# Performance work log

Measured on AMD Instinct MI355X. Metric: run time of the kernel, lower is better.

Reference implementation:

```python
import jax, jax.numpy as jnp
import numpy as np

N_NODES = 50000
N_EDGES = 800000
N_FEAT = 16
N_BASIS = 4
GAMMA = 10.0
R_MAX = 5.0
INV_SQRT2 = 0.7071067811865476


def setup_inputs() -> dict:
    key = jax.random.key(0)
    k1, k2, k3, k4 = jax.random.split(key, 4)
    pos = jax.random.normal(k1, (N_NODES, 3), dtype=jnp.float32)
    node_features = jax.random.normal(k2, (N_NODES, N_FEAT), dtype=jnp.float32)
    # build edges with no self-loops: dst = (src + 1 + r) % N, r in [0, N-2]
    src = jax.random.randint(k3, (N_EDGES,), 0, N_NODES)
    r = jax.random.randint(k4, (N_EDGES,), 0, N_NODES - 1)
    dst = (src + 1 + r) % N_NODES
    edge_idx = jnp.stack([src, dst], axis=0).astype(jnp.int64)
    return {"pos": pos, "node_features": node_features, "edge_idx": edge_idx}


def _gaussian_basis(d):
    # d: [E] -> [E, N_BASIS]
    centers = jnp.linspace(0.0, R_MAX, N_BASIS, dtype=d.dtype)
    return jnp.exp(-GAMMA * (d[:, None] - centers[None, :]) ** 2)


def _pos_to_rep(v):
    # v: [N, 3, C] cartesian along axis -2 -> complex spherical l=1 basis,
    # returned as stacked (real, imag): [2, N, 3, C]
    x, y, z = v[..., 0, :], v[..., 1, :], v[..., 2, :]
    zero = jnp.zeros_like(z)
    real = jnp.stack([x * INV_SQRT2, z, -x * INV_SQRT2], axis=-2)
    imag = jnp.stack([-y * INV_SQRT2, zero, -y * INV_SQRT2], axis=-2)
    return jnp.stack([real, imag], axis=0)


def reference(pos, node_features, edge_idx):
    src, dst = edge_idx[0], edge_idx[1]
    disp = pos[dst] - pos[src]                      # [E, 3]
    dist = jnp.linalg.norm(disp, axis=-1)           # [E]
    bf = _gaussian_basis(dist)                      # [E, B]
    unit = disp / dist[:, None]                     # [E, 3]
    nf = node_features[dst]                         # [E, F]
    # outer products: [E, 3, B, F]
    edge_vals = (unit[:, :, None, None] * bf[:, None, :, None]
                 * nf[:, None, None, :])
    edge_vals = edge_vals.reshape(edge_vals.shape[0], 3, N_BASIS * N_FEAT)
    node_vecs = jax.ops.segment_sum(edge_vals, src, num_segments=N_NODES)  # [N,3,C]
    return _pos_to_rep(node_vecs)
```

## Files before the change

### kernel.cpp

```cpp
#include <hip/hip_runtime.h>

#define N_FEAT 16
#define N_BASIS 4
#define GAMMA 10.0f
#define R_MAX 5.0f
#define INV_SQRT2 0.70710678118654752f

#define BUCKET 50
#define CAP 1088
#define MAXB 1024
#define SC_BLOCK 512
#define SC_EDGES 4096
#define ACC_BLOCK 512

#define FXINV   (1.0f / 2097152.0f)
#define KC      (-GAMMA * 1.4426950408889634f)
#define BIAS21  21.0f

#if __has_builtin(__builtin_amdgcn_exp2f)
#define EXP2(x) __builtin_amdgcn_exp2f(x)
#else
#define EXP2(x) exp2f(x)
#endif

__global__ void bucket_scatter_kernel(const int* __restrict__ src,
                                      const int* __restrict__ dst,
                                      const float* __restrict__ pos,
                                      float4* __restrict__ pos4,
                                      int* __restrict__ gcursor,
                                      int* __restrict__ sorted,
                                      int n_edges, int nbuck, int n_nodes) {
    __shared__ int h[MAXB];
    __shared__ int cur[MAXB];
    __shared__ int gbase[MAXB];
    __shared__ int pay[SC_EDGES];

    int t = threadIdx.x;

    {
        int i = blockIdx.x * SC_BLOCK + t;
        if (i < n_nodes)
            pos4[i] = make_float4(pos[3 * i], pos[3 * i + 1], pos[3 * i + 2], 0.0f);
    }

    int base_e = blockIdx.x * SC_EDGES;
    int nloc = n_edges - base_e;
    if (nloc > SC_EDGES) nloc = SC_EDGES;

    for (int i = t; i < nbuck; i += SC_BLOCK) h[i] = 0;
    __syncthreads();

    unsigned pk[8];
    bool ok[8];
#pragma unroll
    for (int r = 0; r < 8; ++r) {
        int i = t + r * SC_BLOCK;
        ok[r] = (i < nloc);
        unsigned s = ok[r] ? (unsigned)src[base_e + i] : 0u;
        unsigned d = ok[r] ? (unsigned)dst[base_e + i] : 0u;
        pk[r] = (s << 16) | d;
        if (ok[r]) atomicAdd(&h[s / BUCKET], 1);
    }
    __syncthreads();

    if (t < 64) {
        int run = 0;
        for (int base = 0; base < nbuck; base += 64) {
            int i = base + t;
            int v = (i < nbuck) ? h[i] : 0;
            int incl = v;
            for (int off = 1; off < 64; off <<= 1) {
                int y = __shfl_up(incl, off, 64);
                if (t >= off) incl += y;
            }
            if (i < nbuck) h[i] = run + incl - v;
            run += __shfl(incl, 63, 64);
        }
    }
    __syncthreads();
    for (int i = t; i < nbuck; i += SC_BLOCK) cur[i] = h[i];
    __syncthreads();

#pragma unroll
    for (int r = 0; r < 8; ++r) {
        if (ok[r]) {
            int b = (int)((pk[r] >> 16) / BUCKET);
            int p = atomicAdd(&cur[b], 1);
            pay[p] = (int)pk[r];
        }
    }
    __syncthreads();

    for (int b = t; b < nbuck; b += SC_BLOCK) {
        int c = cur[b] - h[b];
        gbase[b] = (c > 0) ? atomicAdd(&gcursor[b], c) : 0;
    }
    __syncthreads();

    for (int i = t; i < nloc; i += SC_BLOCK) {
        unsigned P = (unsigned)pay[i];
        int b = (int)((P >> 16) / BUCKET);
        int idx = gbase[b] + (i - h[b]);
        if (idx < CAP) sorted[b * CAP + idx] = (int)P;
    }
}

__global__ __launch_bounds__(ACC_BLOCK) void accumulate_kernel(
        const float4* __restrict__ pos4,
        const float* __restrict__ nfeat,
        const int* __restrict__ sorted,
        const int* __restrict__ gcursor,
        float* __restrict__ out,
        int n_nodes) {
    __shared__ int acc[BUCKET * 192];
    __shared__ float4 spos[BUCKET];

    int b = blockIdx.x;
    int t = threadIdx.x;
    int w = t >> 6;
    int lane = t & 63;
    int g = lane >> 4;
    int f = lane & 15;
    int nbase = b * BUCKET;

    int4* accv = (int4*)acc;
    for (int i = t; i < BUCKET * 48; i += ACC_BLOCK)
        accv[i] = make_int4(0, 0, 0, 0);
    if (t < BUCKET) {
        int gn = nbase + t;
        spos[t] = (gn < n_nodes) ? pos4[gn] : make_float4(0.f, 0.f, 0.f, 0.f);
    }
    __syncthreads();

    int cnt = gcursor[b];
    if (cnt > CAP) cnt = CAP;
    const int* seg = sorted + b * CAP;

    const int stride = ACC_BLOCK / 64;
    int iters = (cnt + 3) >> 2;

    unsigned E; bool live; int sl; float4 p; float nfv; float4 ps;
    {
        int e = (w << 2) + g;
        live = (e < cnt);
        E = live ? (unsigned)seg[e] : 0u;
        int d = E & 0xFFFF;
        sl = live ? ((int)(E >> 16) - nbase) : 0;
        p = pos4[d];
        nfv = nfeat[(d << 4) + f];
        ps = spos[sl];
    }

    for (int it = w; it < iters; it += stride) {
        unsigned cE = E; bool clive = live; int csl = sl;
        float4 cp = p, cps = ps; float cnf = nfv;

        int nit = it + stride;
        if (nit < iters) {
            int e = (nit << 2) + g;
            live = (e < cnt);
            E = live ? (unsigned)seg[e] : 0u;
            int d = E & 0xFFFF;
            sl = live ? ((int)(E >> 16) - nbase) : 0;
            p = pos4[d];
            nfv = nfeat[(d << 4) + f];
            ps = spos[sl];
        }

        float dx = cp.x - cps.x, dy = cp.y - cps.y, dz = cp.z - cps.z;
        float r2 = dx * dx + dy * dy + dz * dz;
        r2 = clive ? r2 : 1.0f;
        float inv = __builtin_amdgcn_rsqf(r2);
        float dist = r2 * inv;
        float nfi = clive ? cnf * inv : 0.0f;

        int rotbase = f + (csl << 4);
        int sl192 = csl * 192;
#pragma unroll
        for (int kk = 0; kk < N_BASIS; ++kk) {
            float ck = (float)kk * (R_MAX / (N_BASIS - 1));
            float tt = dist - ck;
            float bb = EXP2(fmaf(tt * tt, KC, BIAS21));
            float val = bb * nfi;
            int* ap = acc + sl192 + ((rotbase + (kk << 4)) & 63);
            atomicAdd(ap,       (int)(dx * val));
            atomicAdd(ap + 64,  (int)(dy * val));
            atomicAdd(ap + 128, (int)(dz * val));
        }
    }

    __syncthreads();

    for (int j = w; j < BUCKET; j += stride) {
        int gn = nbase + j;
        if (gn >= n_nodes) continue;
        int rot = (lane + (j << 4)) & 63;
        int jb = j * 192;
        float x = (float)acc[jb + rot] * FXINV;
        float y = (float)acc[jb + 64 + rot] * FXINV;
        float z = (float)acc[jb + 128 + rot] * FXINV;
        size_t obase = (size_t)gn * 192 + lane;
        float* re = out + obase;
        float* im = out + (size_t)n_nodes * 192 + obase;
        float xs = x * INV_SQRT2;
        float ys = -y * INV_SQRT2;
        re[0]   = xs;
        re[64]  = z;
        re[128] = -xs;
        im[0]   = ys;
        im[64]  = 0.0f;
        im[128] = ys;
    }
}

extern "C" void kernel_launch(void* const* d_in, const int* in_sizes, int n_in,
                              void* d_out, int out_size, void* d_ws, size_t ws_size,
                              hipStream_t stream) {
    const float* pos = (const float*)d_in[0];
    const float* nfeat = (const float*)d_in[1];
    const int* edge_idx = (const int*)d_in[2];

    int n_nodes = in_sizes[0] / 3;
    int n_edges = in_sizes[2] / 2;

    const int* src = edge_idx;
    const int* dst = edge_idx + n_edges;

    float* out = (float*)d_out;
    int nbuck = (n_nodes + BUCKET - 1) / BUCKET;

    char* ws = (char*)d_ws;
    size_t o = 0;
    auto alloc = [&](size_t bytes) {
        char* p = ws + o;
        o = (o + bytes + 255) & ~(size_t)255;
        return p;
    };
    int* gcursor = (int*)alloc((size_t)nbuck * 4);
    int* sorted  = (int*)alloc((size_t)nbuck * CAP * 4);
    float4* pos4 = (float4*)alloc((size_t)n_nodes * 16);

    hipMemsetAsync(gcursor, 0, (size_t)nbuck * sizeof(int), stream);

    {
        int grid = (n_edges + SC_EDGES - 1) / SC_EDGES;
        bucket_scatter_kernel<<<grid, SC_BLOCK, 0, stream>>>(src, dst, pos, pos4,
                                                             gcursor, sorted,
                                                             n_edges, nbuck, n_nodes);
    }

    accumulate_kernel<<<nbuck, ACC_BLOCK, 0, stream>>>(pos4, nfeat, sorted, gcursor,
                                                       out, n_nodes);
}
```

Baseline: 66.81 us.

## Replace LDS fixed-point atomics with per-node local sort and register accumulation

Buckets now hold 64 nodes, so bucket indexing becomes a shift. Inside each bucket the accumulate kernel counting-sorts edges by source node in LDS. Each 16-lane group then owns one node and accumulates its 12 outputs in float registers, which removes the fixed-point LDS atomics and the quantization they introduced. The costs are load imbalance from degree variance within a wavefront (loops run to the max degree of four nodes), an extra LDS sort pass, and fewer nodes per block in flight.

```diff
diff --git a/kernel.cpp b/kernel.cpp
--- a/kernel.cpp
+++ b/kernel.cpp
@@ -6,16 +6,15 @@
 #define R_MAX 5.0f
 #define INV_SQRT2 0.70710678118654752f
 
-#define BUCKET 50
-#define CAP 1088
+#define BUCKET 64
+#define CAP 1360
 #define MAXB 1024
 #define SC_BLOCK 512
 #define SC_EDGES 4096
 #define ACC_BLOCK 512
 
-#define FXINV   (1.0f / 2097152.0f)
 #define KC      (-GAMMA * 1.4426950408889634f)
-#define BIAS21  21.0f
+#define CKD     (R_MAX / (N_BASIS - 1))
 
 #if __has_builtin(__builtin_amdgcn_exp2f)
 #define EXP2(x) __builtin_amdgcn_exp2f(x)
@@ -59,7 +58,7 @@
         unsigned s = ok[r] ? (unsigned)src[base_e + i] : 0u;
         unsigned d = ok[r] ? (unsigned)dst[base_e + i] : 0u;
         pk[r] = (s << 16) | d;
-        if (ok[r]) atomicAdd(&h[s / BUCKET], 1);
+        if (ok[r]) atomicAdd(&h[s >> 6], 1);
     }
     __syncthreads();
 
@@ -84,7 +83,7 @@
 #pragma unroll
     for (int r = 0; r < 8; ++r) {
         if (ok[r]) {
-            int b = (int)((pk[r] >> 16) / BUCKET);
+            int b = (int)(pk[r] >> 22);
             int p = atomicAdd(&cur[b], 1);
             pay[p] = (int)pk[r];
         }
@@ -99,7 +98,7 @@
 
     for (int i = t; i < nloc; i += SC_BLOCK) {
         unsigned P = (unsigned)pay[i];
-        int b = (int)((P >> 16) / BUCKET);
+        int b = (int)(P >> 22);
         int idx = gbase[b] + (i - h[b]);
         if (idx < CAP) sorted[b * CAP + idx] = (int)P;
     }
@@ -112,104 +111,140 @@
         const int* __restrict__ gcursor,
         float* __restrict__ out,
         int n_nodes) {
-    __shared__ int acc[BUCKET * 192];
+    __shared__ int spay[CAP + 64];
+    __shared__ int off[BUCKET + 1];
+    __shared__ int cnt[BUCKET];
+    __shared__ int cur[BUCKET];
     __shared__ float4 spos[BUCKET];
 
     int b = blockIdx.x;
     int t = threadIdx.x;
     int w = t >> 6;
     int lane = t & 63;
-    int g = lane >> 4;
+    int grp = lane >> 4;
     int f = lane & 15;
-    int nbase = b * BUCKET;
-
-    int4* accv = (int4*)acc;
-    for (int i = t; i < BUCKET * 48; i += ACC_BLOCK)
-        accv[i] = make_int4(0, 0, 0, 0);
+    int nbase = b << 6;
+
+    int ecnt = gcursor[b];
+    if (ecnt > CAP) ecnt = CAP;
+    const int* seg = sorted + b * CAP;
+
     if (t < BUCKET) {
+        cnt[t] = 0;
         int gn = nbase + t;
         spos[t] = (gn < n_nodes) ? pos4[gn] : make_float4(0.f, 0.f, 0.f, 0.f);
     }
     __syncthreads();
 
-    int cnt = gcursor[b];
-    if (cnt > CAP) cnt = CAP;
-    const int* seg = sorted + b * CAP;
-
-    const int stride = ACC_BLOCK / 64;
-    int iters = (cnt + 3) >> 2;
-
-    unsigned E; bool live; int sl; float4 p; float nfv; float4 ps;
-    {
-        int e = (w << 2) + g;
-        live = (e < cnt);
-        E = live ? (unsigned)seg[e] : 0u;
-        int d = E & 0xFFFF;
-        sl = live ? ((int)(E >> 16) - nbase) : 0;
-        p = pos4[d];
-        nfv = nfeat[(d << 4) + f];
-        ps = spos[sl];
-    }
-
-    for (int it = w; it < iters; it += stride) {
-        unsigned cE = E; bool clive = live; int csl = sl;
-        float4 cp = p, cps = ps; float cnf = nfv;
-
-        int nit = it + stride;
-        if (nit < iters) {
-            int e = (nit << 2) + g;
-            live = (e < cnt);
-            E = live ? (unsigned)seg[e] : 0u;
-            int d = E & 0xFFFF;
-            sl = live ? ((int)(E >> 16) - nbase) : 0;
-            p = pos4[d];
-            nfv = nfeat[(d << 4) + f];
-            ps = spos[sl];
-        }
-
-        float dx = cp.x - cps.x, dy = cp.y - cps.y, dz = cp.z - cps.z;
-        float r2 = dx * dx + dy * dy + dz * dz;
-        r2 = clive ? r2 : 1.0f;
-        float inv = __builtin_amdgcn_rsqf(r2);
-        float dist = r2 * inv;
-        float nfi = clive ? cnf * inv : 0.0f;
-
-        int rotbase = f + (csl << 4);
-        int sl192 = csl * 192;
-#pragma unroll
-        for (int kk = 0; kk < N_BASIS; ++kk) {
-            float ck = (float)kk * (R_MAX / (N_BASIS - 1));
-            float tt = dist - ck;
-            float bb = EXP2(fmaf(tt * tt, KC, BIAS21));
-            float val = bb * nfi;
-            int* ap = acc + sl192 + ((rotbase + (kk << 4)) & 63);
-            atomicAdd(ap,       (int)(dx * val));
-            atomicAdd(ap + 64,  (int)(dy * val));
-            atomicAdd(ap + 128, (int)(dz * val));
-        }
-    }
-
-    __syncthreads();
-
-    for (int j = w; j < BUCKET; j += stride) {
-        int gn = nbase + j;
-        if (gn >= n_nodes) continue;
-        int rot = (lane + (j << 4)) & 63;
-        int jb = j * 192;
-        float x = (float)acc[jb + rot] * FXINV;
-        float y = (float)acc[jb + 64 + rot] * FXINV;
-        float z = (float)acc[jb + 128 + rot] * FXINV;
-        size_t obase = (size_t)gn * 192 + lane;
-        float* re = out + obase;
-        float* im = out + (size_t)n_nodes * 192 + obase;
-        float xs = x * INV_SQRT2;
-        float ys = -y * INV_SQRT2;
-        re[0]   = xs;
-        re[64]  = z;
-        re[128] = -xs;
-        im[0]   = ys;
-        im[64]  = 0.0f;
-        im[128] = ys;
+    for (int i = t; i < ecnt; i += ACC_BLOCK)
+        atomicAdd(&cnt[((unsigned)seg[i] >> 16) & 63], 1);
+    __syncthreads();
+
+    if (t < 64) {
+        int v = cnt[t];
+        int incl = v;
+        for (int o2 = 1; o2 < 64; o2 <<= 1) {
+            int y = __shfl_up(incl, o2, 64);
+            if (t >= o2) incl += y;
+        }
+        off[t + 1] = incl;
+        if (t == 0) off[0] = 0;
+        cur[t] = incl - v;
+    }
+    __syncthreads();
+
+    for (int i = t; i < ecnt; i += ACC_BLOCK) {
+        int E = seg[i];
+        int p = atomicAdd(&cur[((unsigned)E >> 16) & 63], 1);
+        spay[p] = E;
+    }
+    __syncthreads();
+
+    for (int set = 0; set < 2; ++set) {
+        int nl = (w << 3) + (set << 2) + grp;
+        int gn = nbase + nl;
+        int myoff = off[nl];
+        int deg = off[nl + 1] - myoff;
+        float4 ps = spos[nl];
+
+        int m1 = max(deg, __shfl_xor(deg, 16, 64));
+        int maxdeg = max(m1, __shfl_xor(m1, 32, 64));
+
+        float ax0 = 0.f, ax1 = 0.f, ax2 = 0.f, ax3 = 0.f;
+        float ay0 = 0.f, ay1 = 0.f, ay2 = 0.f, ay3 = 0.f;
+        float az0 = 0.f, az1 = 0.f, az2 = 0.f, az3 = 0.f;
+
+        if (maxdeg > 0) {
+            int degm1 = (deg > 0) ? deg - 1 : 0;
+            int E1;
+            float4 p0;
+            float nf0;
+            {
+                int i0 = myoff + 0;
+                int E0 = spay[i0];
+                E1 = spay[myoff + min(1, degm1)];
+                int d0 = (deg > 0) ? (E0 & 0xFFFF) : 0;
+                p0 = pos4[d0];
+                nf0 = nfeat[(d0 << 4) + f];
+            }
+            for (int s = 0; s < maxdeg; ++s) {
+                bool clv = (s < deg);
+                float4 cp = p0;
+                float cnf = nf0;
+
+                int E2 = spay[myoff + min(s + 2, degm1)];
+                int d1 = ((s + 1) < deg) ? (E1 & 0xFFFF) : 0;
+                p0 = pos4[d1];
+                nf0 = nfeat[(d1 << 4) + f];
+                E1 = E2;
+
+                float dx = cp.x - ps.x, dy = cp.y - ps.y, dz = cp.z - ps.z;
+                float r2 = dx * dx + dy * dy + dz * dz;
+                r2 = clv ? r2 : 1.0f;
+                float inv = __builtin_amdgcn_rsqf(r2);
+                float dist = r2 * inv;
+                float nfi = clv ? cnf * inv : 0.0f;
+                float q = dist * dist * KC;
+#define KSTEP(KK, AX, AY, AZ)                                          \
+                {                                                      \
+                    const float ck = (float)(KK) * CKD;                \
+                    const float mk = -2.0f * KC * ck;                  \
+                    const float qk = KC * ck * ck;                     \
+                    float bb = EXP2(fmaf(dist, mk, q + qk));           \
+                    float val = bb * nfi;                              \
+                    AX = fmaf(dx, val, AX);                            \
+                    AY = fmaf(dy, val, AY);                            \
+                    AZ = fmaf(dz, val, AZ);                            \
+                }
+                KSTEP(0, ax0, ay0, az0);
+                KSTEP(1, ax1, ay1, az1);
+                KSTEP(2, ax2, ay2, az2);
+                KSTEP(3, ax3, ay3, az3);
+#undef KSTEP
+            }
+        }
+
+        if (gn < n_nodes) {
+            float* re = out + (size_t)gn * 192;
+            float* im = out + (size_t)n_nodes * 192 + (size_t)gn * 192;
+#define WOUT(KK, AX, AY, AZ)                                           \
+            {                                                          \
+                int o1 = (KK) * 16 + f;                                \
+                float xs = (AX)*INV_SQRT2;                             \
+                float ys = -(AY)*INV_SQRT2;                            \
+                re[o1]       = xs;                                     \
+                re[64 + o1]  = (AZ);                                   \
+                re[128 + o1] = -xs;                                    \
+                im[o1]       = ys;                                     \
+                im[64 + o1]  = 0.0f;                                   \
+                im[128 + o1] = ys;                                     \
+            }
+            WOUT(0, ax0, ay0, az0);
+            WOUT(1, ax1, ay1, az1);
+            WOUT(2, ax2, ay2, az2);
+            WOUT(3, ax3, ay3, az3);
+#undef WOUT
+        }
     }
 }
 
@@ -227,7 +262,7 @@
     const int* dst = edge_idx + n_edges;
 
     float* out = (float*)d_out;
-    int nbuck = (n_nodes + BUCKET - 1) / BUCKET;
+    int nbuck = (n_nodes + 63) >> 6;
 
     char* ws = (char*)d_ws;
     size_t o = 0;
```

Result: faster. 63.89 us (-4.4%).
